# Kernel optimization log

Hardware: AMD Instinct MI355X
Metric: run time of the kernel (lower is better)

Reference implementation:

```python
import jax, jax.numpy as jnp
import numpy as np

THRESH = 6.0   # latent_dist_threshold
SCALE = 1.0    # reward_scale
EPS = 1e-6


def _count_scatter(idx, vals):
    # idx, vals: [B, V, N]; counts[b,v,s] = sum of vals over queries whose argmin == s
    B, V, N = idx.shape
    bi = jnp.arange(B)[:, None, None]
    vi = jnp.arange(V)[None, :, None]
    return jnp.zeros((B, V, N), jnp.int32).at[bi, vi, idx].add(vals)


def _direction(min_dists, min_idx, query_xy, source_xy, query_mask):
    # one chamfer direction: queries matched to nearest source particles
    d = jnp.take_along_axis(source_xy, min_idx[..., None], axis=2)  # [B,V,N,2]
    dist = jnp.linalg.norm(query_xy - d, ord=2, axis=-1)            # [B,V,N]
    latent_mask = min_dists > THRESH
    rpm = query_mask | latent_mask                                   # reward_particle_mask
    vals = jnp.where(rpm, 0, 1).astype(jnp.int32)
    count = _count_scatter(min_idx, vals)                            # density counts per source
    w = 1.0 / (jnp.take_along_axis(count, min_idx, axis=2).astype(jnp.float32) + EPS)
    dist = jnp.where(rpm, 0.0, w * dist)
    unmatched = jnp.any((~query_mask) & latent_mask, axis=-1).astype(jnp.float32)
    groups = jnp.maximum(jnp.sum(count > 0, axis=2).astype(jnp.float32) + unmatched, 1.0)
    return -(jnp.sum(dist, axis=2) + unmatched) / groups             # [B,V]


def setup_inputs() -> dict:
    key = jax.random.key(0)
    k1, k2 = jax.random.split(key)
    achieved = jax.random.normal(k1, (256, 2, 512, 10), dtype=jnp.float32)
    desired = jax.random.normal(k2, (256, 2, 512, 10), dtype=jnp.float32)
    return {"achieved": achieved, "desired": desired}


def reference(achieved, desired):
    # latent_classifier=None -> obj_class_cond = ones -> mask = (ones == 0) = all False
    state_mask = jnp.zeros(achieved.shape[:-1], bool)
    goal_mask = jnp.zeros(desired.shape[:-1], bool)
    s_vis = achieved[..., 5:9]
    s_xy = achieved[..., :2]
    g_vis = desired[..., 5:9]
    g_xy = desired[..., :2]
    # 'l2_simple' pairwise squared dist: P[b,v,i,j] = ||s_vis_i - g_vis_j||^2
    P = (jnp.sum(s_vis ** 2, -1)[..., :, None]
         + jnp.sum(g_vis ** 2, -1)[..., None, :]
         - 2.0 * jnp.einsum('bvnd,bvmd->bvnm', s_vis, g_vis))
    P = jnp.where(state_mask[..., :, None] | goal_mask[..., None, :], jnp.inf, P)
    # goal -> state: min over state axis (2)
    md1 = jnp.min(P, axis=2)
    mi1 = jnp.argmin(P, axis=2).astype(jnp.int32)
    r_g2s = _direction(md1, mi1, g_xy, s_xy, goal_mask)
    # state -> goal: min over goal axis (3)
    md2 = jnp.min(P, axis=3)
    mi2 = jnp.argmin(P, axis=3).astype(jnp.int32)
    r_s2g = _direction(md2, mi2, s_xy, g_xy, state_mask)
    rv = (r_g2s + r_s2g) / 2.0                                       # [B,V]
    no_valid = jnp.all(goal_mask, -1) | jnp.all(state_mask, -1)
    rv = jnp.where(no_valid, -1.0, rv)
    reward = jnp.mean(rv, axis=1)
    return SCALE * reward[:, None]                                    # [B,1]
```

## Files before the change

kernel.cpp:

```cpp
#include <hip/hip_runtime.h>
#include <math.h>

#define NB 256
#define NV 2
#define NN 512
#define ND 10
#define THRESH_SQ 6.0f
#define EPS_W 1e-6f

typedef __attribute__((ext_vector_type(8))) short bf16x8;
typedef __attribute__((ext_vector_type(4))) float f32x4;

__device__ __forceinline__ unsigned short f2bf(float x) {
    union { float f; unsigned u; } v; v.f = x;
    unsigned r = v.u + 0x7FFFu + ((v.u >> 16) & 1u);
    return (unsigned short)(r >> 16);
}
__device__ __forceinline__ float bf2f(unsigned short h) {
    union { unsigned u; float f; } v; v.u = ((unsigned)h) << 16; return v.f;
}
__device__ __forceinline__ void split3(float x, unsigned short* s) {
    unsigned short h = f2bf(x); float r = x - bf2f(h);
    unsigned short m = f2bf(r); float r2 = r - bf2f(m);
    s[0] = h; s[1] = m; s[2] = f2bf(r2);
}
__device__ __forceinline__ unsigned umin_(unsigned a, unsigned b) { return a < b ? a : b; }

__device__ __forceinline__ int recaddr(int c, int row) {
    return (c << 13) + ((row << 4) ^ (c << 5));
}

__global__ __launch_bounds__(1024, 4)
void chamfer_bv(const float* __restrict__ achieved,
                const float* __restrict__ desired,
                float* __restrict__ rv_out)
{
    const int bv  = blockIdx.x;
    const int tid = threadIdx.x;

    __shared__ __align__(16) char bufA[32768];
    __shared__ __align__(16) char bufB[32768];
    __shared__ __align__(16) unsigned colKey[NN * 4];

    const unsigned short ONE = 0x3F80;

    if (tid < NN) {
        const int pi[6] = {0,0,1,2,1,0};
        const float* arow = achieved + ((size_t)bv * NN + tid) * ND;
        float a5 = arow[5], a6 = arow[6], a7 = arow[7], a8 = arow[8];
        unsigned short us[4][3];
        split3(-2.0f*a5, us[0]); split3(-2.0f*a6, us[1]);
        split3(-2.0f*a7, us[2]); split3(-2.0f*a8, us[3]);
        float sn2 = a5*a5 + a6*a6 + a7*a7 + a8*a8;
        unsigned short sn[3]; split3(sn2, sn);
        unsigned short t[32];
        #pragma unroll
        for (int d = 0; d < 4; ++d)
            #pragma unroll
            for (int p = 0; p < 6; ++p)
                t[d*6+p] = us[d][pi[p]];
        t[24]=sn[0]; t[25]=sn[1]; t[26]=sn[2];
        t[27]=ONE;   t[28]=ONE;   t[29]=ONE;
        t[30]=ONE;   t[31]=0;
        #pragma unroll
        for (int c = 0; c < 4; ++c) {
            bf16x8 v;
            #pragma unroll
            for (int e = 0; e < 8; ++e) v[e] = (short)t[c*8+e];
            *(bf16x8*)(bufA + recaddr(c, tid)) = v;
        }
    } else {
        const int pj[6] = {0,1,0,0,1,2};
        const int r = tid - NN;
        const float* drow = desired + ((size_t)bv * NN + r) * ND;
        float g5 = drow[5], g6 = drow[6], g7 = drow[7], g8 = drow[8];
        unsigned short gs[4][3];
        split3(g5, gs[0]); split3(g6, gs[1]); split3(g7, gs[2]); split3(g8, gs[3]);
        float gn2 = g5*g5 + g6*g6 + g7*g7 + g8*g8;
        unsigned short gn[3]; split3(gn2, gn);
        unsigned short t[32];
        #pragma unroll
        for (int d = 0; d < 4; ++d)
            #pragma unroll
            for (int p = 0; p < 6; ++p)
                t[d*6+p] = gs[d][pj[p]];
        t[24]=ONE;   t[25]=ONE;   t[26]=ONE;
        t[27]=gn[0]; t[28]=gn[1]; t[29]=gn[2];
        t[30]=0x3A80; t[31]=0;
        #pragma unroll
        for (int c = 0; c < 4; ++c) {
            bf16x8 v;
            #pragma unroll
            for (int e = 0; e < 8; ++e) v[e] = (short)t[c*8+e];
            *(bf16x8*)(bufB + recaddr(c, r)) = v;
        }
    }
    colKey[tid]        = 0xFFFFFFFFu;
    colKey[tid + 1024] = 0xFFFFFFFFu;
    __syncthreads();

    const int lane = tid & 63, wid = tid >> 6;
    const int lrow = lane & 15, lchk = lane >> 4;

    bf16x8 afr[2];
    #pragma unroll
    for (int nt = 0; nt < 2; ++nt)
        afr[nt] = *(const bf16x8*)(bufA + recaddr(lchk, (wid<<5) + (nt<<4) + lrow));

    unsigned rowKey[2][4];
    int ncst[2][4];
    #pragma unroll
    for (int nt = 0; nt < 2; ++nt)
        #pragma unroll
        for (int j = 0; j < 4; ++j) {
            rowKey[nt][j] = 0xFFFFFFFFu;
            ncst[nt][j]   = (wid<<5) + (nt<<4) + (lchk<<2) + j;
        }

    const unsigned MASK = 0xFFFFFE00u;
    const f32x4 z = {0.0f, 0.0f, 0.0f, 0.0f};

    bf16x8 bfr = *(const bf16x8*)(bufB + recaddr(lchk, lrow));
    #pragma unroll 4
    for (int mt = 0; mt < 32; ++mt) {
        const int mtn = (mt + 1) & 31;
        bf16x8 bnext = *(const bf16x8*)(bufB + recaddr(lchk, (mtn<<4) + lrow));
        const unsigned mcur = (unsigned)((mt<<4) + lrow);
        unsigned cp0, cp1;
        #pragma unroll
        for (int nt = 0; nt < 2; ++nt) {
            f32x4 acc = __builtin_amdgcn_mfma_f32_16x16x32_bf16(afr[nt], bfr, z, 0, 0, 0);
            unsigned b0 = __float_as_uint(acc[0]) & MASK;
            unsigned b1 = __float_as_uint(acc[1]) & MASK;
            unsigned b2 = __float_as_uint(acc[2]) & MASK;
            unsigned b3 = __float_as_uint(acc[3]) & MASK;
            rowKey[nt][0] = umin_(rowKey[nt][0], b0 | mcur);
            rowKey[nt][1] = umin_(rowKey[nt][1], b1 | mcur);
            rowKey[nt][2] = umin_(rowKey[nt][2], b2 | mcur);
            rowKey[nt][3] = umin_(rowKey[nt][3], b3 | mcur);
            unsigned k0 = b0 | (unsigned)ncst[nt][0];
            unsigned k1 = b1 | (unsigned)ncst[nt][1];
            unsigned k2 = b2 | (unsigned)ncst[nt][2];
            unsigned k3 = b3 | (unsigned)ncst[nt][3];
            unsigned cp = umin_(umin_(k0, k1), umin_(k2, k3));
            if (nt == 0) cp0 = cp; else cp1 = cp;
        }
        unsigned cv = umin_(cp0, cp1);
        atomicMin(&colKey[(mcur << 2) | lchk], cv);
        bfr = bnext;
    }

    #pragma unroll
    for (int nt = 0; nt < 2; ++nt) {
        #pragma unroll
        for (int j = 0; j < 4; ++j) {
            unsigned v = rowKey[nt][j];
            #pragma unroll
            for (int s = 1; s <= 8; s <<= 1)
                v = umin_(v, (unsigned)__shfl_xor((int)v, s));
            rowKey[nt][j] = v;
        }
    }
    __syncthreads();

    unsigned* rowKeyArr = (unsigned*)bufA;
    int*      cnt       = (int*)(bufA + 2048);
    float*    redF      = (float*)(bufA + 4096);
    int*      redI      = (int*)(bufA + 4224);

    if (lrow == 0) {
        #pragma unroll
        for (int nt = 0; nt < 2; ++nt)
            #pragma unroll
            for (int j = 0; j < 4; ++j)
                rowKeyArr[ncst[nt][j]] = rowKey[nt][j];
    }
    if (tid < NN) cnt[tid] = 0;
    __syncthreads();

    float sumA = 0.0f, sumB = 0.0f;
    int grpPk = 0, latPk = 0;
    int miA = 0, miB = 0;
    bool latA = false, latB = false;
    if (tid < NN) {
        const uint4 ck = *(const uint4*)&colKey[tid << 2];
        const unsigned kA = umin_(umin_(ck.x, ck.y), umin_(ck.z, ck.w));
        const unsigned kB = rowKeyArr[tid];
        miA = (int)(kA & 0x1FFu);
        miB = (int)(kB & 0x1FFu);
        latA = __uint_as_float(kA & MASK) > THRESH_SQ;
        latB = __uint_as_float(kB & MASK) > THRESH_SQ;
        if (!latA) atomicAdd(&cnt[miA], 1);
        if (!latB) atomicAdd(&cnt[miB], 0x10000);
    }
    __syncthreads();

    if (tid < NN) {
        const float* arow_e = achieved + ((size_t)bv * NN + tid) * ND;
        const float* drow_e = desired  + ((size_t)bv * NN + tid) * ND;
        if (!latA) {
            const float* sp = achieved + ((size_t)bv * NN + miA) * ND;
            float dx = drow_e[0] - sp[0], dy = drow_e[1] - sp[1];
            float w = 1.0f / ((float)(cnt[miA] & 0xFFFF) + EPS_W);
            sumA = w * sqrtf(dx*dx + dy*dy);
        }
        if (!latB) {
            const float* gp = desired + ((size_t)bv * NN + miB) * ND;
            float dx = arow_e[0] - gp[0], dy = arow_e[1] - gp[1];
            float w = 1.0f / ((float)(((unsigned)cnt[miB]) >> 16) + EPS_W);
            sumB = w * sqrtf(dx*dx + dy*dy);
        }
        const int c0i = cnt[tid];
        grpPk = ((c0i & 0xFFFF) ? 1 : 0) | ((((unsigned)c0i) >> 16) ? 0x10000 : 0);
        latPk = (latA ? 1 : 0) | (latB ? 2 : 0);
    }

    #pragma unroll
    for (int off = 32; off > 0; off >>= 1) {
        sumA  += __shfl_down(sumA, off);
        sumB  += __shfl_down(sumB, off);
        grpPk += __shfl_down(grpPk, off);
        latPk |= __shfl_down(latPk, off);
    }
    if (lane == 0) {
        redF[wid*2] = sumA; redF[wid*2+1] = sumB;
        redI[wid*2] = grpPk; redI[wid*2+1] = latPk;
    }
    __syncthreads();
    if (tid == 0) {
        float sA = 0.0f, sB = 0.0f; int G = 0, L = 0;
        #pragma unroll
        for (int w2 = 0; w2 < 16; ++w2) {
            sA += redF[w2*2]; sB += redF[w2*2+1];
            G  += redI[w2*2]; L |= redI[w2*2+1];
        }
        float unmA = (L & 1) ? 1.0f : 0.0f;
        float unmB = (L & 2) ? 1.0f : 0.0f;
        float gA = (float)(G & 0xFFFF), gB = (float)(((unsigned)G) >> 16);
        float rA = -(sA + unmA) / fmaxf(gA + unmA, 1.0f);
        float rB = -(sB + unmB) / fmaxf(gB + unmB, 1.0f);
        rv_out[bv] = 0.5f * (rA + rB);
    }
}

__global__ void chamfer_finalize(const float* __restrict__ rv, float* __restrict__ out)
{
    int b = blockIdx.x * 256 + threadIdx.x;
    if (b < NB) out[b] = 0.5f * (rv[2*b] + rv[2*b + 1]);
}

extern "C" void kernel_launch(void* const* d_in, const int* in_sizes, int n_in,
                              void* d_out, int out_size, void* d_ws, size_t ws_size,
                              hipStream_t stream)
{
    const float* achieved = (const float*)d_in[0];
    const float* desired  = (const float*)d_in[1];
    float* out = (float*)d_out;
    float* rv  = (float*)d_ws;

    chamfer_bv<<<NB * NV, 1024, 0, stream>>>(achieved, desired, rv);
    chamfer_finalize<<<1, 256, 0, stream>>>(rv, out);
}
```

Before: 30.76 us.

## Retile MFMA work as 64 rows by 256 columns per wave, drop row shuffles

Measured after the change: 32.87 us. 6.9% more time.

```diff
diff --git a/kernel.cpp b/kernel.cpp
--- a/kernel.cpp
+++ b/kernel.cpp
@@ -101,34 +101,36 @@
 
     const int lane = tid & 63, wid = tid >> 6;
     const int lrow = lane & 15, lchk = lane >> 4;
-
-    bf16x8 afr[2];
+    const int rg = wid & 7;
+    const int tg = wid >> 3;
+
+    bf16x8 afr[4];
     #pragma unroll
-    for (int nt = 0; nt < 2; ++nt)
-        afr[nt] = *(const bf16x8*)(bufA + recaddr(lchk, (wid<<5) + (nt<<4) + lrow));
-
-    unsigned rowKey[2][4];
-    int ncst[2][4];
+    for (int nt = 0; nt < 4; ++nt)
+        afr[nt] = *(const bf16x8*)(bufA + recaddr(lchk, (rg<<6) + (nt<<4) + lrow));
+
+    unsigned rowKey[4][4];
+    int ncst[4][4];
     #pragma unroll
-    for (int nt = 0; nt < 2; ++nt)
+    for (int nt = 0; nt < 4; ++nt)
         #pragma unroll
         for (int j = 0; j < 4; ++j) {
             rowKey[nt][j] = 0xFFFFFFFFu;
-            ncst[nt][j]   = (wid<<5) + (nt<<4) + (lchk<<2) + j;
+            ncst[nt][j]   = (rg<<6) + (nt<<4) + (lchk<<2) + j;
         }
 
     const unsigned MASK = 0xFFFFFE00u;
     const f32x4 z = {0.0f, 0.0f, 0.0f, 0.0f};
 
-    bf16x8 bfr = *(const bf16x8*)(bufB + recaddr(lchk, lrow));
+    bf16x8 bfr = *(const bf16x8*)(bufB + recaddr(lchk, (tg<<8) + lrow));
     #pragma unroll 4
-    for (int mt = 0; mt < 32; ++mt) {
-        const int mtn = (mt + 1) & 31;
-        bf16x8 bnext = *(const bf16x8*)(bufB + recaddr(lchk, (mtn<<4) + lrow));
-        const unsigned mcur = (unsigned)((mt<<4) + lrow);
-        unsigned cp0, cp1;
-        #pragma unroll
-        for (int nt = 0; nt < 2; ++nt) {
+    for (int t = 0; t < 16; ++t) {
+        const int tn = (t + 1) & 15;
+        bf16x8 bnext = *(const bf16x8*)(bufB + recaddr(lchk, (tg<<8) + (tn<<4) + lrow));
+        const unsigned mcur = (unsigned)(((tg<<4) + t)<<4) + (unsigned)lrow;
+        unsigned cp0, cp1, cp2, cp3;
+        #pragma unroll
+        for (int nt = 0; nt < 4; ++nt) {
             f32x4 acc = __builtin_amdgcn_mfma_f32_16x16x32_bf16(afr[nt], bfr, z, 0, 0, 0);
             unsigned b0 = __float_as_uint(acc[0]) & MASK;
             unsigned b1 = __float_as_uint(acc[1]) & MASK;
@@ -143,40 +145,37 @@
             unsigned k2 = b2 | (unsigned)ncst[nt][2];
             unsigned k3 = b3 | (unsigned)ncst[nt][3];
             unsigned cp = umin_(umin_(k0, k1), umin_(k2, k3));
-            if (nt == 0) cp0 = cp; else cp1 = cp;
-        }
-        unsigned cv = umin_(cp0, cp1);
+            if (nt == 0) cp0 = cp; else if (nt == 1) cp1 = cp;
+            else if (nt == 2) cp2 = cp; else cp3 = cp;
+        }
+        unsigned cv = umin_(umin_(cp0, cp1), umin_(cp2, cp3));
         atomicMin(&colKey[(mcur << 2) | lchk], cv);
         bfr = bnext;
     }
-
-    #pragma unroll
-    for (int nt = 0; nt < 2; ++nt) {
-        #pragma unroll
-        for (int j = 0; j < 4; ++j) {
-            unsigned v = rowKey[nt][j];
-            #pragma unroll
-            for (int s = 1; s <= 8; s <<= 1)
-                v = umin_(v, (unsigned)__shfl_xor((int)v, s));
-            rowKey[nt][j] = v;
-        }
-    }
-    __syncthreads();
-
-    unsigned* rowKeyArr = (unsigned*)bufA;
-    int*      cnt       = (int*)(bufA + 2048);
-    float*    redF      = (float*)(bufA + 4096);
-    int*      redI      = (int*)(bufA + 4224);
-
-    if (lrow == 0) {
-        #pragma unroll
-        for (int nt = 0; nt < 2; ++nt)
+    __syncthreads();
+
+    unsigned* rowKeyS = (unsigned*)bufB;
+    int* cnt = (int*)(bufA + 2048);
+    if (tg == 0) {
+        #pragma unroll
+        for (int nt = 0; nt < 4; ++nt)
             #pragma unroll
             for (int j = 0; j < 4; ++j)
-                rowKeyArr[ncst[nt][j]] = rowKey[nt][j];
+                rowKeyS[(ncst[nt][j] << 4) + lrow] = rowKey[nt][j];
     }
     if (tid < NN) cnt[tid] = 0;
     __syncthreads();
+    if (tg == 1) {
+        #pragma unroll
+        for (int nt = 0; nt < 4; ++nt)
+            #pragma unroll
+            for (int j = 0; j < 4; ++j)
+                atomicMin(&rowKeyS[(ncst[nt][j] << 4) + lrow], rowKey[nt][j]);
+    }
+    __syncthreads();
+
+    float* redF = (float*)(bufA + 4096);
+    int*   redI = (int*)(bufA + 4224);
 
     float sumA = 0.0f, sumB = 0.0f;
     int grpPk = 0, latPk = 0;
@@ -185,7 +184,12 @@
     if (tid < NN) {
         const uint4 ck = *(const uint4*)&colKey[tid << 2];
         const unsigned kA = umin_(umin_(ck.x, ck.y), umin_(ck.z, ck.w));
-        const unsigned kB = rowKeyArr[tid];
+        const uint4* rs = (const uint4*)&rowKeyS[tid << 4];
+        const uint4 r0 = rs[0], r1 = rs[1], r2 = rs[2], r3 = rs[3];
+        unsigned kB = umin_(umin_(umin_(r0.x, r0.y), umin_(r0.z, r0.w)),
+                            umin_(umin_(r1.x, r1.y), umin_(r1.z, r1.w)));
+        kB = umin_(kB, umin_(umin_(umin_(r2.x, r2.y), umin_(r2.z, r2.w)),
+                             umin_(umin_(r3.x, r3.y), umin_(r3.z, r3.w))));
         miA = (int)(kA & 0x1FFu);
         miB = (int)(kB & 0x1FFu);
         latA = __uint_as_float(kA & MASK) > THRESH_SQ;
```
